# Kernel optimization log

Hardware: AMD Instinct MI355X
Metric: run time of the kernel (lower is better)

Reference implementation:

```python
import jax, jax.numpy as jnp
import numpy as np

B = 16384          # batch
S = 510            # no_of_states
D = 2 * S + 4      # 1024, context width
HID = 512          # self.hidden_size
H = 1024           # no_of_heads
INHIB = 3.0        # kWTA inhibition coefficient


def _lin(x, W, b):
    # torch nn.Linear convention: W is [out, in]
    return x @ W.T + b


def kwta(x, kw):
    """Per-row dynamic-k winner-take-all.
    k_i = argmax(kw[i]); top-k entries of x[i] kept, the rest divided by INHIB.
    Vectorized replacement for the original per-row topk + scatter loop."""
    k = jnp.argmax(kw, axis=1)                         # [B] per-row k
    s = -jnp.sort(-x, axis=1)                          # descending sort per row
    idx = jnp.clip(k - 1, 0, x.shape[1] - 1)
    thr = jnp.take_along_axis(s, idx[:, None], axis=1)  # k-th largest value
    mask = (x >= thr) & (k[:, None] > 0)               # winners (k=0 -> none)
    return jnp.where(mask, x, x / INHIB)


def setup_inputs() -> dict:
    key = jax.random.key(0)
    ks = jax.random.split(key, 30)

    def n(k, shape, s=0.02):
        return (jax.random.normal(k, shape) * s).astype(jnp.float32)

    return {
        "input": jax.random.normal(ks[0], (B, S), jnp.float32),
        "task_indicator": jax.random.normal(ks[1], (B, S + 4), jnp.float32),
        "hidden": jax.random.normal(ks[2], (1, B, D), jnp.float32),
        # Elman RNN step (single layer, hidden width D)
        "w_ih": n(ks[3], (D, D)), "b_ih": n(ks[4], (D,)),
        "w_hh": n(ks[5], (D, D)), "b_hh": n(ks[6], (D,)),
        # context gating heads
        "w_cx11": n(ks[7], (2 * HID, D)), "b_cx11": n(ks[8], (2 * HID,)),
        "w_cx12": n(ks[9], (2 * HID, 2 * HID)), "b_cx12": n(ks[10], (2 * HID,)),
        "w_cx21": n(ks[11], (HID, D)), "b_cx21": n(ks[12], (HID,)),
        "w_cx22": n(ks[13], (HID, HID)), "b_cx22": n(ks[14], (HID,)),
        "w_cx31": n(ks[15], (H, D)), "b_cx31": n(ks[16], (H,)),
        "w_cx32": n(ks[17], (H, H)), "b_cx32": n(ks[18], (H,)),
        # main MLP stack
        "w_l1": n(ks[19], (2 * HID, D)), "b_l1": n(ks[20], (2 * HID,)),
        "w_l2": n(ks[21], (HID, 2 * HID)), "b_l2": n(ks[22], (HID,)),
        "w_l3": n(ks[23], (H, HID)), "b_l3": n(ks[24], (H,)),
        "w_l4": n(ks[25], (H, H)), "b_l4": n(ks[26], (H,)),
    }


def reference(input, task_indicator, hidden,
              w_ih, b_ih, w_hh, b_hh,
              w_cx11, b_cx11, w_cx12, b_cx12,
              w_cx21, b_cx21, w_cx22, b_cx22,
              w_cx31, b_cx31, w_cx32, b_cx32,
              w_l1, b_l1, w_l2, b_l2, w_l3, b_l3, w_l4, b_l4):
    ctx = jnp.concatenate([input, task_indicator], axis=1)      # [B, D]
    h0 = hidden[0]                                              # [B, D]
    # Elman RNN step: out == next hidden state
    out = jnp.tanh(ctx @ w_ih.T + b_ih + h0 @ w_hh.T + b_hh)    # [B, D]
    next_hidden = out[:, None, :]                               # transpose(0,1) of [1,B,D]

    cx1 = jax.nn.softmax(_lin(jnp.tanh(_lin(out, w_cx11, b_cx11)), w_cx12, b_cx12), axis=1)
    cx2 = jax.nn.softmax(_lin(jnp.tanh(_lin(out, w_cx21, b_cx21)), w_cx22, b_cx22), axis=1)
    cx3 = jax.nn.softmax(_lin(jnp.tanh(_lin(out, w_cx31, b_cx31)), w_cx32, b_cx32), axis=1)

    x = _lin(out, w_l1, b_l1)        # [B, 2*HID]
    x = kwta(x, cx1)
    x = _lin(x, w_l2, b_l2)          # [B, HID]
    x = kwta(x, cx2)
    x = _lin(x, w_l3, b_l3)          # [B, H]
    x = kwta(x, cx3)
    x = _lin(x, w_l4, b_l4)          # [B, H]
    return (x, next_hidden)
```

## Files before the change

kernel.cpp:

```cpp
#include <hip/hip_runtime.h>
#include <math.h>

#define BB 16384
#define BM 128
#define BN 128
#define BK 32

typedef float f32x2 __attribute__((ext_vector_type(2)));

__global__ __launch_bounds__(256) void concat_kernel(const float* __restrict__ inp,
    const float* __restrict__ task, float* __restrict__ ctx)
{
  int idx = blockIdx.x * 256 + threadIdx.x;
  int b = idx >> 10;
  int c = idx & 1023;
  float v;
  if (c < 510) v = inp[(size_t)b * 510 + c];
  else         v = task[(size_t)b * 514 + (c - 510)];
  ctx[idx] = v;
}

template<bool TANH, bool CIN>
__global__ __launch_bounds__(256) void gemm32g_kernel(
    const float* __restrict__ A, const float* __restrict__ W,
    const float* __restrict__ b1, const float* __restrict__ b2,
    const float* __restrict__ Cin, float* __restrict__ C,
    int N, int K, int lda, int ldw, unsigned foldmask)
{
  __shared__ float As[BK * BM];
  __shared__ float Bs[BK * BN];
  const int tid = threadIdx.x;
  const int tx = tid & 15;
  const int ty = tid >> 4;
  const int gx = gridDim.x;
  const int nwg = gx * gridDim.y;
  const int flat = blockIdx.y * gx + blockIdx.x;
  const int cpx = nwg >> 3;
  const int swb = (flat & 7) * cpx + (flat >> 3);
  const int m0 = (swb / gx) * BM;
  const int n0 = (swb % gx) * BN;
  const int rrow = tid >> 3;
  const int kc = (tid & 7) << 2;

  f32x2 res[2][2][4][2], cur[2][2][4][2];
#pragma unroll
  for (int g = 0; g < 2; ++g)
#pragma unroll
    for (int h = 0; h < 2; ++h)
#pragma unroll
      for (int i = 0; i < 4; ++i)
#pragma unroll
        for (int jp = 0; jp < 2; ++jp) {
          res[g][h][i][jp] = (f32x2){0.f, 0.f};
          cur[g][h][i][jp] = (f32x2){0.f, 0.f};
        }

  float4 ra[4], rb[4];
  const int NT = K / BK;

#pragma unroll
  for (int i = 0; i < 4; ++i) {
    int r = rrow + (i << 5);
    ra[i] = *(const float4*)(A + (size_t)(m0 + r) * lda + kc);
    rb[i] = *(const float4*)(W + (size_t)(n0 + r) * ldw + kc);
  }

  for (int kt = 0; kt < NT; ++kt) {
    __syncthreads();
#pragma unroll
    for (int i = 0; i < 4; ++i) {
      int cS = (rrow + (i << 5)) ^ kc;
      As[(kc + 0) * BM + cS] = ra[i].x;
      As[(kc + 1) * BM + cS] = ra[i].y;
      As[(kc + 2) * BM + cS] = ra[i].z;
      As[(kc + 3) * BM + cS] = ra[i].w;
      Bs[(kc + 0) * BN + cS] = rb[i].x;
      Bs[(kc + 1) * BN + cS] = rb[i].y;
      Bs[(kc + 2) * BN + cS] = rb[i].z;
      Bs[(kc + 3) * BN + cS] = rb[i].w;
    }
    __syncthreads();
    if (kt + 1 < NT) {
      int kb = (kt + 1) * BK;
#pragma unroll
      for (int i = 0; i < 4; ++i) {
        int r = rrow + (i << 5);
        ra[i] = *(const float4*)(A + (size_t)(m0 + r) * lda + kb + kc);
        rb[i] = *(const float4*)(W + (size_t)(n0 + r) * ldw + kb + kc);
      }
    }
#pragma unroll 8
    for (int kk = 0; kk < BK; ++kk) {
      const int swz = kk & 28;
      const float4 a0 = *(const float4*)&As[kk * BM + ((4 * ty) ^ swz)];
      const float4 a1 = *(const float4*)&As[kk * BM + 64 + ((4 * ty) ^ swz)];
      const float4 b0 = *(const float4*)&Bs[kk * BN + ((4 * tx) ^ swz)];
      const float4 b1r = *(const float4*)&Bs[kk * BN + 64 + ((4 * tx) ^ swz)];
      const float av[2][4] = {{a0.x, a0.y, a0.z, a0.w}, {a1.x, a1.y, a1.z, a1.w}};
      const f32x2 wv2[2][2] = {{(f32x2){b0.x, b0.y}, (f32x2){b0.z, b0.w}},
                               {(f32x2){b1r.x, b1r.y}, (f32x2){b1r.z, b1r.w}}};
#pragma unroll
      for (int g = 0; g < 2; ++g)
#pragma unroll
        for (int i = 0; i < 4; ++i) {
          const f32x2 as = (f32x2){av[g][i], av[g][i]};
#pragma unroll
          for (int h = 0; h < 2; ++h)
#pragma unroll
            for (int jp = 0; jp < 2; ++jp)
              cur[g][h][i][jp] =
                  __builtin_elementwise_fma(as, wv2[h][jp], cur[g][h][i][jp]);
        }
    }
    if ((foldmask >> kt) & 1u) {
#pragma unroll
      for (int g = 0; g < 2; ++g)
#pragma unroll
        for (int h = 0; h < 2; ++h)
#pragma unroll
          for (int i = 0; i < 4; ++i)
#pragma unroll
            for (int jp = 0; jp < 2; ++jp) {
              res[g][h][i][jp] = res[g][h][i][jp] + cur[g][h][i][jp];
              cur[g][h][i][jp] = (f32x2){0.f, 0.f};
            }
    }
  }

  float4 b1v[2], b2v[2];
#pragma unroll
  for (int h = 0; h < 2; ++h) {
    int cb = n0 + h * 64 + 4 * tx;
    b1v[h] = b1 ? *(const float4*)&b1[cb] : make_float4(0.f, 0.f, 0.f, 0.f);
    b2v[h] = (CIN && b2) ? *(const float4*)&b2[cb] : make_float4(0.f, 0.f, 0.f, 0.f);
  }
#pragma unroll
  for (int g = 0; g < 2; ++g)
#pragma unroll
    for (int i = 0; i < 4; ++i) {
      int row = m0 + g * 64 + 4 * ty + i;
#pragma unroll
      for (int h = 0; h < 2; ++h) {
        int col = n0 + h * 64 + 4 * tx;
        const float rs[4] = {res[g][h][i][0][0], res[g][h][i][0][1],
                             res[g][h][i][1][0], res[g][h][i][1][1]};
        float4 o;
        if (CIN) {
          float4 ci = *(const float4*)&Cin[(size_t)row * N + col];
          o.x = ((ci.x + b1v[h].x) + rs[0]) + b2v[h].x;
          o.y = ((ci.y + b1v[h].y) + rs[1]) + b2v[h].y;
          o.z = ((ci.z + b1v[h].z) + rs[2]) + b2v[h].z;
          o.w = ((ci.w + b1v[h].w) + rs[3]) + b2v[h].w;
        } else if (b1) {
          o.x = rs[0] + b1v[h].x;
          o.y = rs[1] + b1v[h].y;
          o.z = rs[2] + b1v[h].z;
          o.w = rs[3] + b1v[h].w;
        } else {
          o.x = rs[0]; o.y = rs[1]; o.z = rs[2]; o.w = rs[3];
        }
        if (TANH) {
          o.x = (float)tanh((double)o.x);
          o.y = (float)tanh((double)o.y);
          o.z = (float)tanh((double)o.z);
          o.w = (float)tanh((double)o.w);
        }
        *(float4*)&C[(size_t)row * N + col] = o;
      }
    }
}

template<int NELEM>
__global__ __launch_bounds__(256) void kwta_kernel(const float* __restrict__ x,
    const float* __restrict__ cxz, float* __restrict__ out)
{
  constexpr int NPER = NELEM / 256;
  const int row = blockIdx.x;
  const int tid = threadIdx.x;
  const float* xr = x + (size_t)row * NELEM;
  const float* zr = cxz + (size_t)row * NELEM;
  float* orow = out + (size_t)row * NELEM;

  __shared__ float es[NELEM];
  __shared__ float red[256];
  __shared__ int   ri[256];
  __shared__ float bs[8];
  __shared__ float ssum;
  __shared__ unsigned hist[256];
  __shared__ unsigned cum[256];
  __shared__ int selBin;
  __shared__ unsigned selBase;

  float zv[NPER];
  float mx = -INFINITY;
#pragma unroll
  for (int j = 0; j < NPER; ++j) {
    zv[j] = zr[tid + (j << 8)];
    mx = fmaxf(mx, zv[j]);
  }
  red[tid] = mx;
  __syncthreads();
  for (int s = 128; s > 0; s >>= 1) {
    if (tid < s) red[tid] = fmaxf(red[tid], red[tid + s]);
    __syncthreads();
  }
  mx = red[0];
  __syncthreads();

  float ev[NPER];
#pragma unroll
  for (int j = 0; j < NPER; ++j) {
    float d = zv[j] - mx;
    ev[j] = (float)exp((double)d);
    es[tid + (j << 8)] = ev[j];
  }
  __syncthreads();

  if (tid < NELEM / 128) {
    const float* a = &es[tid * 128];
    float r0 = a[0], r1 = a[1], r2 = a[2], r3 = a[3];
    float r4 = a[4], r5 = a[5], r6 = a[6], r7 = a[7];
    for (int i = 8; i < 128; i += 8) {
      r0 += a[i + 0]; r1 += a[i + 1]; r2 += a[i + 2]; r3 += a[i + 3];
      r4 += a[i + 4]; r5 += a[i + 5]; r6 += a[i + 6]; r7 += a[i + 7];
    }
    bs[tid] = ((r0 + r1) + (r2 + r3)) + ((r4 + r5) + (r6 + r7));
  }
  __syncthreads();
  if (tid == 0) {
    float s;
    if (NELEM == 1024)
      s = ((bs[0] + bs[1]) + (bs[2] + bs[3])) + ((bs[4] + bs[5]) + (bs[6] + bs[7]));
    else
      s = (bs[0] + bs[1]) + (bs[2] + bs[3]);
    ssum = s;
  }
  __syncthreads();
  const float s = ssum;

  float bv = -INFINITY; int bi = 0x7fffffff;
#pragma unroll
  for (int j = 0; j < NPER; ++j) {
    float u = ev[j] / s;
    int i = tid + (j << 8);
    if (u > bv) { bv = u; bi = i; }
  }
  red[tid] = bv; ri[tid] = bi;
  __syncthreads();
  for (int st = 128; st > 0; st >>= 1) {
    if (tid < st) {
      float ov = red[tid + st]; int oi = ri[tid + st];
      if (ov > red[tid] || (ov == red[tid] && oi < ri[tid])) { red[tid] = ov; ri[tid] = oi; }
    }
    __syncthreads();
  }
  const int k = ri[0];

  float xv[NPER]; unsigned key[NPER];
#pragma unroll
  for (int j = 0; j < NPER; ++j) {
    float v = xr[tid + (j << 8)];
    xv[j] = v;
    unsigned sb = __float_as_uint(v);
    key[j] = (sb & 0x80000000u) ? ~sb : (sb | 0x80000000u);
  }

  float thr = 0.f;
  const bool kzero = (k == 0);
  if (!kzero) {
    unsigned ur = (unsigned)(NELEM - k);
    unsigned prefix = 0, pmask = 0;
    for (int shift = 24; shift >= 0; shift -= 8) {
      hist[tid] = 0;
      __syncthreads();
#pragma unroll
      for (int j = 0; j < NPER; ++j)
        if ((key[j] & pmask) == prefix) atomicAdd(&hist[(key[j] >> shift) & 255u], 1u);
      __syncthreads();
      unsigned v = hist[tid];
      cum[tid] = v;
      __syncthreads();
      for (int d = 1; d < 256; d <<= 1) {
        unsigned t = (tid >= d) ? cum[tid - d] : 0u;
        __syncthreads();
        v += t; cum[tid] = v;
        __syncthreads();
      }
      unsigned excl = v - hist[tid];
      if (ur >= excl && ur < v) { selBin = tid; selBase = excl; }
      __syncthreads();
      prefix |= ((unsigned)selBin) << shift;
      pmask  |= (255u << shift);
      ur -= selBase;
      __syncthreads();
    }
    thr = (prefix & 0x80000000u) ? __uint_as_float(prefix & 0x7FFFFFFFu)
                                 : __uint_as_float(~prefix);
  }
#pragma unroll
  for (int j = 0; j < NPER; ++j) {
    float v = xv[j];
    bool keep = !kzero && (v >= thr);
    orow[tid + (j << 8)] = keep ? v : (v / 3.0f);
  }
}

extern "C" void kernel_launch(void* const* d_in, const int* in_sizes, int n_in,
                              void* d_out, int out_size, void* d_ws, size_t ws_size,
                              hipStream_t stream) {
  const float* input  = (const float*)d_in[0];
  const float* task   = (const float*)d_in[1];
  const float* hidden = (const float*)d_in[2];
  const float* w_ih   = (const float*)d_in[3];  const float* b_ih   = (const float*)d_in[4];
  const float* w_hh   = (const float*)d_in[5];  const float* b_hh   = (const float*)d_in[6];
  const float* w_cx11 = (const float*)d_in[7];  const float* b_cx11 = (const float*)d_in[8];
  const float* w_cx12 = (const float*)d_in[9];  const float* b_cx12 = (const float*)d_in[10];
  const float* w_cx21 = (const float*)d_in[11]; const float* b_cx21 = (const float*)d_in[12];
  const float* w_cx22 = (const float*)d_in[13]; const float* b_cx22 = (const float*)d_in[14];
  const float* w_cx31 = (const float*)d_in[15]; const float* b_cx31 = (const float*)d_in[16];
  const float* w_cx32 = (const float*)d_in[17]; const float* b_cx32 = (const float*)d_in[18];
  const float* w_l1   = (const float*)d_in[19]; const float* b_l1   = (const float*)d_in[20];
  const float* w_l2   = (const float*)d_in[21]; const float* b_l2   = (const float*)d_in[22];
  const float* w_l3   = (const float*)d_in[23]; const float* b_l3   = (const float*)d_in[24];
  const float* w_l4   = (const float*)d_in[25]; const float* b_l4   = (const float*)d_in[26];

  float* out_x = (float*)d_out;
  float* out_h = out_x + (size_t)BB * 1024;

  int R = BB;
  while ((size_t)R * 8192 > ws_size && R > 128) R >>= 1;
  const int nChunks = BB / R;

  const unsigned FM1024 = (1u << 11) | (1u << 23) | (1u << 31);
  const unsigned FM512  = (1u << 11) | (1u << 15);

  dim3 blk(256);

  concat_kernel<<<BB * 1024 / 256, blk, 0, stream>>>(input, task, out_x);

  for (int c = 0; c < nChunks; ++c) {
    const size_t r0 = (size_t)c * R;
    float* S0 = (float*)d_ws;
    float* S1 = S0 + (size_t)R * 1024;
    float* S1hi = S1 + (size_t)R * 512;
    float* OX = out_x + r0 * 1024;
    const float* ctx_c = OX;
    const float* hid_c = hidden + r0 * 1024;
    float* out_c = out_h + r0 * 1024;
    dim3 g1024(1024 / BN, R / BM);
    dim3 g512 ( 512 / BN, R / BM);

    gemm32g_kernel<false, false><<<g1024, blk, 0, stream>>>(
        ctx_c, w_ih, nullptr, nullptr, nullptr, S0, 1024, 1024, 1024, 1024, FM1024);
    gemm32g_kernel<true, true><<<g1024, blk, 0, stream>>>(
        hid_c, w_hh, b_ih, b_hh, S0, out_c, 1024, 1024, 1024, 1024, FM1024);
    gemm32g_kernel<true, false><<<g1024, blk, 0, stream>>>(
        out_c, w_cx11, b_cx11, nullptr, nullptr, S1, 1024, 1024, 1024, 1024, FM1024);
    gemm32g_kernel<false, false><<<g1024, blk, 0, stream>>>(
        S1, w_cx12, b_cx12, nullptr, nullptr, S0, 1024, 1024, 1024, 1024, FM1024);
    gemm32g_kernel<false, false><<<g1024, blk, 0, stream>>>(
        out_c, w_l1, b_l1, nullptr, nullptr, OX, 1024, 1024, 1024, 1024, FM1024);
    kwta_kernel<1024><<<R, blk, 0, stream>>>(OX, S0, OX);
    gemm32g_kernel<true, false><<<g512, blk, 0, stream>>>(
        out_c, w_cx21, b_cx21, nullptr, nullptr, S1, 512, 1024, 1024, 1024, FM1024);
    gemm32g_kernel<false, false><<<g512, blk, 0, stream>>>(
        S1, w_cx22, b_cx22, nullptr, nullptr, S1hi, 512, 512, 512, 512, FM512);
    gemm32g_kernel<false, false><<<g512, blk, 0, stream>>>(
        OX, w_l2, b_l2, nullptr, nullptr, S0, 512, 1024, 1024, 1024, FM1024);
    kwta_kernel<512><<<R, blk, 0, stream>>>(S0, S1hi, S0);
    gemm32g_kernel<true, false><<<g1024, blk, 0, stream>>>(
        out_c, w_cx31, b_cx31, nullptr, nullptr, S1, 1024, 1024, 1024, 1024, FM1024);
    gemm32g_kernel<false, false><<<g1024, blk, 0, stream>>>(
        S1, w_cx32, b_cx32, nullptr, nullptr, OX, 1024, 1024, 1024, 1024, FM1024);
    gemm32g_kernel<false, false><<<g1024, blk, 0, stream>>>(
        S0, w_l3, b_l3, nullptr, nullptr, S1, 1024, 512, 512, 512, FM512);
    kwta_kernel<1024><<<R, blk, 0, stream>>>(S1, OX, S1);
    gemm32g_kernel<false, false><<<g1024, blk, 0, stream>>>(
        S1, w_l4, b_l4, nullptr, nullptr, OX, 1024, 1024, 1024, 1024, FM1024);
  }
}
```

Baseline: 4.528 ms.

## Double-buffer shared memory and register-prefetch LDS fragments in fp32 GEMM

```diff
diff --git a/kernel.cpp b/kernel.cpp
--- a/kernel.cpp
+++ b/kernel.cpp
@@ -21,14 +21,14 @@
 }
 
 template<bool TANH, bool CIN>
-__global__ __launch_bounds__(256) void gemm32g_kernel(
+__global__ __launch_bounds__(256, 2) void gemm32g_kernel(
     const float* __restrict__ A, const float* __restrict__ W,
     const float* __restrict__ b1, const float* __restrict__ b2,
     const float* __restrict__ Cin, float* __restrict__ C,
     int N, int K, int lda, int ldw, unsigned foldmask)
 {
-  __shared__ float As[BK * BM];
-  __shared__ float Bs[BK * BN];
+  __shared__ float As[2][BK * BM];
+  __shared__ float Bs[2][BK * BN];
   const int tid = threadIdx.x;
   const int tx = tid & 15;
   const int ty = tid >> 4;
@@ -58,59 +58,76 @@
   float4 ra[4], rb[4];
   const int NT = K / BK;
 
-#pragma unroll
-  for (int i = 0; i < 4; ++i) {
-    int r = rrow + (i << 5);
-    ra[i] = *(const float4*)(A + (size_t)(m0 + r) * lda + kc);
-    rb[i] = *(const float4*)(W + (size_t)(n0 + r) * ldw + kc);
-  }
-
-  for (int kt = 0; kt < NT; ++kt) {
-    __syncthreads();
+  auto loadG = [&](int kt) {
+    int kb = kt * BK;
+#pragma unroll
+    for (int i = 0; i < 4; ++i) {
+      int r = rrow + (i << 5);
+      ra[i] = *(const float4*)(A + (size_t)(m0 + r) * lda + kb + kc);
+      rb[i] = *(const float4*)(W + (size_t)(n0 + r) * ldw + kb + kc);
+    }
+  };
+  auto stage = [&](int p) {
 #pragma unroll
     for (int i = 0; i < 4; ++i) {
       int cS = (rrow + (i << 5)) ^ kc;
-      As[(kc + 0) * BM + cS] = ra[i].x;
-      As[(kc + 1) * BM + cS] = ra[i].y;
-      As[(kc + 2) * BM + cS] = ra[i].z;
-      As[(kc + 3) * BM + cS] = ra[i].w;
-      Bs[(kc + 0) * BN + cS] = rb[i].x;
-      Bs[(kc + 1) * BN + cS] = rb[i].y;
-      Bs[(kc + 2) * BN + cS] = rb[i].z;
-      Bs[(kc + 3) * BN + cS] = rb[i].w;
-    }
-    __syncthreads();
+      As[p][(kc + 0) * BM + cS] = ra[i].x;
+      As[p][(kc + 1) * BM + cS] = ra[i].y;
+      As[p][(kc + 2) * BM + cS] = ra[i].z;
+      As[p][(kc + 3) * BM + cS] = ra[i].w;
+      Bs[p][(kc + 0) * BN + cS] = rb[i].x;
+      Bs[p][(kc + 1) * BN + cS] = rb[i].y;
+      Bs[p][(kc + 2) * BN + cS] = rb[i].z;
+      Bs[p][(kc + 3) * BN + cS] = rb[i].w;
+    }
+  };
+
+  loadG(0);
+  stage(0);
+  __syncthreads();
+  if (NT > 1) loadG(1);
+
+  for (int kt = 0; kt < NT; ++kt) {
+    const int p = kt & 1;
     if (kt + 1 < NT) {
-      int kb = (kt + 1) * BK;
-#pragma unroll
-      for (int i = 0; i < 4; ++i) {
-        int r = rrow + (i << 5);
-        ra[i] = *(const float4*)(A + (size_t)(m0 + r) * lda + kb + kc);
-        rb[i] = *(const float4*)(W + (size_t)(n0 + r) * ldw + kb + kc);
+      stage(p ^ 1);
+      if (kt + 2 < NT) loadG(kt + 2);
+    }
+    {
+      const float* Ap = As[p];
+      const float* Bp = Bs[p];
+      float4 a0f[2], a1f[2], b0f[2], b1f[2];
+      a0f[0] = *(const float4*)&Ap[(4 * ty)];
+      a1f[0] = *(const float4*)&Ap[64 + (4 * ty)];
+      b0f[0] = *(const float4*)&Bp[(4 * tx)];
+      b1f[0] = *(const float4*)&Bp[64 + (4 * tx)];
+#pragma unroll
+      for (int kk = 0; kk < BK; ++kk) {
+        const int q = kk & 1;
+        if (kk + 1 < BK) {
+          const int swz = (kk + 1) & 28;
+          a0f[q ^ 1] = *(const float4*)&Ap[(kk + 1) * BM + ((4 * ty) ^ swz)];
+          a1f[q ^ 1] = *(const float4*)&Ap[(kk + 1) * BM + 64 + ((4 * ty) ^ swz)];
+          b0f[q ^ 1] = *(const float4*)&Bp[(kk + 1) * BN + ((4 * tx) ^ swz)];
+          b1f[q ^ 1] = *(const float4*)&Bp[(kk + 1) * BN + 64 + ((4 * tx) ^ swz)];
+        }
+        const float av[2][4] = {{a0f[q].x, a0f[q].y, a0f[q].z, a0f[q].w},
+                                {a1f[q].x, a1f[q].y, a1f[q].z, a1f[q].w}};
+        const f32x2 wv2[2][2] = {{(f32x2){b0f[q].x, b0f[q].y}, (f32x2){b0f[q].z, b0f[q].w}},
+                                 {(f32x2){b1f[q].x, b1f[q].y}, (f32x2){b1f[q].z, b1f[q].w}}};
+#pragma unroll
+        for (int g = 0; g < 2; ++g)
+#pragma unroll
+          for (int i = 0; i < 4; ++i) {
+            const f32x2 as = (f32x2){av[g][i], av[g][i]};
+#pragma unroll
+            for (int h = 0; h < 2; ++h)
+#pragma unroll
+              for (int jp = 0; jp < 2; ++jp)
+                cur[g][h][i][jp] =
+                    __builtin_elementwise_fma(as, wv2[h][jp], cur[g][h][i][jp]);
+          }
       }
-    }
-#pragma unroll 8
-    for (int kk = 0; kk < BK; ++kk) {
-      const int swz = kk & 28;
-      const float4 a0 = *(const float4*)&As[kk * BM + ((4 * ty) ^ swz)];
-      const float4 a1 = *(const float4*)&As[kk * BM + 64 + ((4 * ty) ^ swz)];
-      const float4 b0 = *(const float4*)&Bs[kk * BN + ((4 * tx) ^ swz)];
-      const float4 b1r = *(const float4*)&Bs[kk * BN + 64 + ((4 * tx) ^ swz)];
-      const float av[2][4] = {{a0.x, a0.y, a0.z, a0.w}, {a1.x, a1.y, a1.z, a1.w}};
-      const f32x2 wv2[2][2] = {{(f32x2){b0.x, b0.y}, (f32x2){b0.z, b0.w}},
-                               {(f32x2){b1r.x, b1r.y}, (f32x2){b1r.z, b1r.w}}};
-#pragma unroll
-      for (int g = 0; g < 2; ++g)
-#pragma unroll
-        for (int i = 0; i < 4; ++i) {
-          const f32x2 as = (f32x2){av[g][i], av[g][i]};
-#pragma unroll
-          for (int h = 0; h < 2; ++h)
-#pragma unroll
-            for (int jp = 0; jp < 2; ++jp)
-              cur[g][h][i][jp] =
-                  __builtin_elementwise_fma(as, wv2[h][jp], cur[g][h][i][jp]);
-        }
     }
     if ((foldmask >> kt) & 1u) {
 #pragma unroll
@@ -125,6 +142,7 @@
               cur[g][h][i][jp] = (f32x2){0.f, 0.f};
             }
     }
+    __syncthreads();
   }
 
   float4 b1v[2], b2v[2];
```

Result: faster. 4.360 ms (-3.7%).
